# Kernel tuning notes

Hardware: AMD Instinct MI355X
Metric: run time of the kernel (lower is better)

## Reference

```python
import jax, jax.numpy as jnp
import numpy as np

N_NODES, N_EDGES = 50000, 800000
NODE_DIM, EDGE_DIM, HIDDEN, NUM_LAYERS = 64, 32, 64, 2
IN_MSG = NODE_DIM + EDGE_DIM  # 96
IN_UPD = NODE_DIM + HIDDEN    # 128


def setup_inputs() -> dict:
    key = jax.random.key(0)
    ks = jax.random.split(key, 12)
    def w(k, shape, fan_in):
        return jax.random.normal(k, shape, jnp.float32) * (1.0 / np.sqrt(fan_in))
    return {
        "node_features": jax.random.normal(ks[0], (N_NODES, NODE_DIM), jnp.float32),
        "edge_features": jax.random.normal(ks[1], (N_EDGES, EDGE_DIM), jnp.float32),
        "msg_w1": w(ks[2], (NUM_LAYERS, IN_MSG, HIDDEN), IN_MSG),
        "msg_b1": w(ks[3], (NUM_LAYERS, HIDDEN), IN_MSG),
        "msg_w2": w(ks[4], (NUM_LAYERS, HIDDEN, HIDDEN), HIDDEN),
        "msg_b2": w(ks[5], (NUM_LAYERS, HIDDEN), HIDDEN),
        "upd_w1": w(ks[6], (IN_UPD, HIDDEN), IN_UPD),
        "upd_b1": w(ks[7], (HIDDEN,), IN_UPD),
        "upd_w2": w(ks[8], (HIDDEN, NODE_DIM), HIDDEN),
        "upd_b2": w(ks[9], (NODE_DIM,), HIDDEN),
        "src": jax.random.randint(ks[10], (N_EDGES,), 0, N_NODES, dtype=jnp.int32),
        "dst": jax.random.randint(ks[11], (N_EDGES,), 0, N_NODES, dtype=jnp.int32),
    }


def reference(node_features, edge_features, msg_w1, msg_b1, msg_w2, msg_b2,
              upd_w1, upd_b1, upd_w2, upd_b2, src, dst):
    n_nodes = node_features.shape[0]
    # message: concat gathered source node feats with edge feats -> [E, node+edge]
    combined = jnp.concatenate([node_features[src], edge_features], axis=-1)
    # sum over the num_layers small Linear-ReLU-Linear message networks
    msg = jnp.zeros((combined.shape[0], msg_w2.shape[-1]), combined.dtype)
    for l in range(msg_w1.shape[0]):  # small fixed num_layers
        h = jax.nn.relu(combined @ msg_w1[l] + msg_b1[l])
        msg = msg + (h @ msg_w2[l] + msg_b2[l])
    # scatter-sum messages to destination nodes, normalize by neighbor count
    agg = jax.ops.segment_sum(msg, dst, num_segments=n_nodes)
    deg = jax.ops.segment_sum(jnp.ones((dst.shape[0],), msg.dtype), dst, num_segments=n_nodes)
    agg = agg / (deg[:, None] + 1e-8)
    # update MLP on concat(node, aggregated)
    comb2 = jnp.concatenate([node_features, agg], axis=-1)
    return jax.nn.relu(comb2 @ upd_w1 + upd_b1) @ upd_w2 + upd_b2
```

## Files before the change

kernel.cpp:

```cpp
#include <hip/hip_runtime.h>
#include <hip/hip_bf16.h>

#define NN 50000
#define NE 800000
#define ND 64
#define ED 32
#define HID 64
#define NL 2
#define IN_MSG 96
#define IN_UPD 128

#define W1_LD 104
#define MSG_LD 72
#define UPD_LD 136

#define NBLK 512
#define WPB 4
#define TOTW (NBLK * WPB)
#define NGRP (NE / 32)
#define NB_SCAN 196

typedef __attribute__((ext_vector_type(8))) short short8;
typedef __attribute__((ext_vector_type(4))) float f32x4;

__device__ inline ushort bf16r(float f) {
    __hip_bfloat16 h = __float2bfloat16(f);
    return *reinterpret_cast<ushort*>(&h);
}
__device__ inline float b2f(unsigned u) {
    union { unsigned u; float f; } x; x.u = u << 16; return x.f;
}
__device__ inline short8 pk8(float4 a, float4 b) {
    short8 r;
    r[0] = (short)bf16r(a.x); r[1] = (short)bf16r(a.y);
    r[2] = (short)bf16r(a.z); r[3] = (short)bf16r(a.w);
    r[4] = (short)bf16r(b.x); r[5] = (short)bf16r(b.y);
    r[6] = (short)bf16r(b.z); r[7] = (short)bf16r(b.w);
    return r;
}
__device__ inline uint2 pack4(float4 v) {
    return make_uint2((unsigned)bf16r(v.x) | ((unsigned)bf16r(v.y) << 16),
                      (unsigned)bf16r(v.z) | ((unsigned)bf16r(v.w) << 16));
}
__device__ inline uint2 pkacc(f32x4 a) {
    return make_uint2((unsigned)bf16r(a[0]) | ((unsigned)bf16r(a[1]) << 16),
                      (unsigned)bf16r(a[2]) | ((unsigned)bf16r(a[3]) << 16));
}

__global__ __launch_bounds__(256) void hist_kernel(const int* __restrict__ dst,
                                                   int* __restrict__ cnt)
{
    const int i = blockIdx.x * 256 + threadIdx.x;
    atomicAdd(&cnt[dst[i]], 1);
}

__global__ __launch_bounds__(256) void scanA_kernel(const int* __restrict__ cnt,
                                                    int* __restrict__ off,
                                                    int* __restrict__ bsum)
{
    __shared__ int buf[256];
    const int t = threadIdx.x;
    const int i = blockIdx.x * 256 + t;
    const int v = (i < NN) ? cnt[i] : 0;
    buf[t] = v;
    __syncthreads();
    #pragma unroll
    for (int d = 1; d < 256; d <<= 1) {
        const int x = (t >= d) ? buf[t - d] : 0;
        __syncthreads();
        buf[t] += x;
        __syncthreads();
    }
    if (i < NN) off[i] = buf[t] - v;
    if (t == 255) bsum[blockIdx.x] = buf[255];
}

__global__ __launch_bounds__(256) void scanB_kernel(int* __restrict__ bsum)
{
    __shared__ int buf[256];
    const int t = threadIdx.x;
    buf[t] = (t < NB_SCAN) ? bsum[t] : 0;
    __syncthreads();
    #pragma unroll
    for (int d = 1; d < 256; d <<= 1) {
        const int x = (t >= d) ? buf[t - d] : 0;
        __syncthreads();
        buf[t] += x;
        __syncthreads();
    }
    if (t < NB_SCAN) bsum[t] = buf[t];
}

__global__ __launch_bounds__(256) void scanC_kernel(const int* __restrict__ bsum,
                                                    int* __restrict__ off,
                                                    int* __restrict__ cursor)
{
    const int b = blockIdx.x;
    const int i = b * 256 + threadIdx.x;
    const int boff = (b > 0) ? bsum[b - 1] : 0;
    if (i < NN) {
        const int e = off[i] + boff;
        off[i] = e;
        cursor[i] = e;
    }
    if (i == 0) off[NN] = NE;
}

__global__ __launch_bounds__(256) void fill_kernel(const int* __restrict__ src,
                                                   const int* __restrict__ dst,
                                                   int* __restrict__ cursor,
                                                   int4* __restrict__ esd,
                                                   float4* __restrict__ agg4)
{
    const int i = blockIdx.x * 256 + threadIdx.x;
    const int d = dst[i];
    const int pos = atomicAdd(&cursor[d], 1);
    esd[pos] = make_int4(i, src[i], d, 0);
    agg4[i] = make_float4(0.f, 0.f, 0.f, 0.f);
}

template <int SORTED>
__global__ __launch_bounds__(256, 2)
void msg_kernel(const float* __restrict__ nf,
                const float* __restrict__ ef,
                const float* __restrict__ w1,
                const float* __restrict__ b1,
                const float* __restrict__ w2,
                const float* __restrict__ b2,
                const int* __restrict__ src,
                const int* __restrict__ dst,
                const int4* __restrict__ esd,
                float* __restrict__ agg,
                float* __restrict__ deg)
{
    __shared__ __align__(16) ushort sW1t[NL][64][W1_LD];
    __shared__ __align__(16) ushort sMS[WPB][32][MSG_LD];
    __shared__ __align__(16) float sB1f[NL][64];
    __shared__ __align__(16) float sB2f[64];

    const int tid = threadIdx.x;
    const int w  = tid >> 6;
    const int l  = tid & 63;
    const int lr = l & 15;
    const int lg = l >> 4;

    {
        const int k16 = tid >> 4, n0 = (tid & 15) * 4;
        #pragma unroll
        for (int lay = 0; lay < NL; ++lay)
            #pragma unroll
            for (int it = 0; it < 6; ++it) {
                const int k = k16 + 16 * it;
                const float4 v = *reinterpret_cast<const float4*>(
                    w1 + ((size_t)lay * IN_MSG + k) * HID + n0);
                sW1t[lay][n0 + 0][k] = bf16r(v.x);
                sW1t[lay][n0 + 1][k] = bf16r(v.y);
                sW1t[lay][n0 + 2][k] = bf16r(v.z);
                sW1t[lay][n0 + 3][k] = bf16r(v.w);
            }
        if (tid < NL * 64) sB1f[tid >> 6][tid & 63] = b1[tid];
        if (tid < 64) sB2f[tid] = b2[tid] + b2[HID + tid];
    }
    short8 w2f[NL][4][2];
    #pragma unroll
    for (int lay = 0; lay < NL; ++lay)
        #pragma unroll
        for (int nt = 0; nt < 4; ++nt)
            #pragma unroll
            for (int ks = 0; ks < 2; ++ks) {
                short8 t;
                #pragma unroll
                for (int j = 0; j < 8; ++j)
                    t[j] = (short)bf16r(
                        w2[((size_t)lay * HID + ks * 32 + 8 * lg + j) * HID + nt * 16 + lr]);
                w2f[lay][nt][ks] = t;
            }
    __syncthreads();

    const float4* nfr = reinterpret_cast<const float4*>(nf);
    const float4* efr = reinterpret_cast<const float4*>(ef);

    int g = blockIdx.x * WPB + w;
    int ev = 0, sv = 0, dv = 0;
    int en = 0, sn = 0, dn = 0;
    if (l < 32) {
        if (SORTED) { const int4 t = esd[(size_t)g * 32 + l]; ev = t.x; sv = t.y; dv = t.z; }
        else        { sv = src[(size_t)g * 32 + l]; dv = dst[(size_t)g * 32 + l]; }
    }
    {
        const int gn = g + TOTW;
        if (gn < NGRP && l < 32) {
            if (SORTED) { const int4 t = esd[(size_t)gn * 32 + l]; en = t.x; sn = t.y; dn = t.z; }
            else        { sn = src[(size_t)gn * 32 + l]; dn = dst[(size_t)gn * 32 + l]; }
        }
    }
    float4 nfv[2][4], efv[2][2];
    #pragma unroll
    for (int mt = 0; mt < 2; ++mt) {
        const int s = __shfl(sv, mt * 16 + lr);
        const float4* p = nfr + (size_t)s * 16;
        nfv[mt][0] = p[2 * lg];     nfv[mt][1] = p[2 * lg + 1];
        nfv[mt][2] = p[8 + 2 * lg]; nfv[mt][3] = p[9 + 2 * lg];
        const int e = SORTED ? __shfl(ev, mt * 16 + lr) : (g * 32 + mt * 16 + lr);
        const float4* q = efr + (size_t)e * 8;
        efv[mt][0] = q[2 * lg];
        efv[mt][1] = q[2 * lg + 1];
    }

    #pragma unroll 1
    while (g < NGRP) {
        const int gn  = g + TOTW;
        const int gnn = g + 2 * TOTW;
        const bool more = (gn < NGRP);

        short8 cmbA[2][3];
        #pragma unroll
        for (int mt = 0; mt < 2; ++mt) {
            cmbA[mt][0] = pk8(nfv[mt][0], nfv[mt][1]);
            cmbA[mt][1] = pk8(nfv[mt][2], nfv[mt][3]);
            cmbA[mt][2] = pk8(efv[mt][0], efv[mt][1]);
        }

        int en2 = 0, sn2 = 0, dn2 = 0;
        if (gnn < NGRP && l < 32) {
            if (SORTED) { const int4 t = esd[(size_t)gnn * 32 + l]; en2 = t.x; sn2 = t.y; dn2 = t.z; }
            else        { sn2 = src[(size_t)gnn * 32 + l]; dn2 = dst[(size_t)gnn * 32 + l]; }
        }
        float4 nfn[2][4], efn[2][2];
        if (more) {
            #pragma unroll
            for (int mt = 0; mt < 2; ++mt) {
                const int e = SORTED ? __shfl(en, mt * 16 + lr) : (gn * 32 + mt * 16 + lr);
                const float4* q = efr + (size_t)e * 8;
                efn[mt][0] = q[2 * lg];
                efn[mt][1] = q[2 * lg + 1];
                const int s = __shfl(sn, mt * 16 + lr);
                const float4* p = nfr + (size_t)s * 16;
                nfn[mt][0] = p[2 * lg];     nfn[mt][1] = p[2 * lg + 1];
                nfn[mt][2] = p[8 + 2 * lg]; nfn[mt][3] = p[9 + 2 * lg];
            }
        }

        f32x4 msg[2][4];
        #pragma unroll
        for (int nt = 0; nt < 4; ++nt) {
            const f32x4 b2v = *reinterpret_cast<const f32x4*>(&sB2f[nt * 16 + 4 * lg]);
            msg[0][nt] = b2v;
            msg[1][nt] = b2v;
        }

        #pragma unroll
        for (int lay = 0; lay < NL; ++lay) {
            f32x4 acc[2][4];
            #pragma unroll
            for (int nt = 0; nt < 4; ++nt) {
                const f32x4 bv = *reinterpret_cast<const f32x4*>(&sB1f[lay][nt * 16 + 4 * lg]);
                acc[0][nt] = bv;
                acc[1][nt] = bv;
            }
            __builtin_amdgcn_s_setprio(1);
            #pragma unroll
            for (int ks = 0; ks < 3; ++ks)
                #pragma unroll
                for (int nt = 0; nt < 4; ++nt) {
                    const short8 Bw = *reinterpret_cast<const short8*>(
                        &sW1t[lay][nt * 16 + lr][ks * 32 + 8 * lg]);
                    acc[0][nt] = __builtin_amdgcn_mfma_f32_16x16x32_bf16(Bw, cmbA[0][ks], acc[0][nt], 0, 0, 0);
                    acc[1][nt] = __builtin_amdgcn_mfma_f32_16x16x32_bf16(Bw, cmbA[1][ks], acc[1][nt], 0, 0, 0);
                }
            __builtin_amdgcn_s_setprio(0);
            #pragma unroll
            for (int mt = 0; mt < 2; ++mt)
                #pragma unroll
                for (int nt = 0; nt < 4; ++nt) {
                    f32x4 a = acc[mt][nt];
                    a[0] = fmaxf(a[0], 0.0f); a[1] = fmaxf(a[1], 0.0f);
                    a[2] = fmaxf(a[2], 0.0f); a[3] = fmaxf(a[3], 0.0f);
                    *reinterpret_cast<uint2*>(&sMS[w][mt * 16 + lr][nt * 16 + 4 * lg]) = pkacc(a);
                }
            short8 hA[2][2];
            #pragma unroll
            for (int mt = 0; mt < 2; ++mt)
                #pragma unroll
                for (int ks = 0; ks < 2; ++ks)
                    hA[mt][ks] = *reinterpret_cast<const short8*>(
                        &sMS[w][mt * 16 + lr][ks * 32 + 8 * lg]);
            __builtin_amdgcn_s_setprio(1);
            #pragma unroll
            for (int ks = 0; ks < 2; ++ks)
                #pragma unroll
                for (int nt = 0; nt < 4; ++nt) {
                    msg[0][nt] = __builtin_amdgcn_mfma_f32_16x16x32_bf16(w2f[lay][nt][ks], hA[0][ks], msg[0][nt], 0, 0, 0);
                    msg[1][nt] = __builtin_amdgcn_mfma_f32_16x16x32_bf16(w2f[lay][nt][ks], hA[1][ks], msg[1][nt], 0, 0, 0);
                }
            __builtin_amdgcn_s_setprio(0);
        }

        #pragma unroll
        for (int mt = 0; mt < 2; ++mt)
            #pragma unroll
            for (int nt = 0; nt < 4; ++nt)
                *reinterpret_cast<uint2*>(&sMS[w][mt * 16 + lr][nt * 16 + 4 * lg]) = pkacc(msg[mt][nt]);

        if (SORTED) {
            float acc = 0.0f;
            int dr = __builtin_amdgcn_readlane(dv, 0);
            #pragma unroll
            for (int r = 0; r < 32; ++r) {
                acc += b2f((unsigned)sMS[w][r][l]);
                const int drn = (r < 31) ? __builtin_amdgcn_readlane(dv, r + 1) : -1;
                if (r == 31 || dr != drn) {
                    atomicAdd(&agg[(size_t)dr * HID + l], acc);
                    acc = 0.0f;
                }
                dr = drn;
            }
        } else {
            #pragma unroll
            for (int r = 0; r < 32; ++r) {
                const int dr = __builtin_amdgcn_readlane(dv, r);
                atomicAdd(&agg[(size_t)dr * HID + l], b2f((unsigned)sMS[w][r][l]));
            }
            if (l < 32) atomicAdd(&deg[dv], 1.0f);
        }

        ev = en; sv = sn; dv = dn;
        en = en2; sn = sn2; dn = dn2;
        #pragma unroll
        for (int mt = 0; mt < 2; ++mt) {
            #pragma unroll
            for (int i = 0; i < 4; ++i) nfv[mt][i] = nfn[mt][i];
            efv[mt][0] = efn[mt][0]; efv[mt][1] = efn[mt][1];
        }
        g = gn;
    }
}

template <int USE_OFF>
__global__ __launch_bounds__(128, 2)
void node_update_kernel(const float* __restrict__ nf,
                        const float* __restrict__ agg,
                        const int* __restrict__ off,
                        const float* __restrict__ degf,
                        const float* __restrict__ uw1,
                        const float* __restrict__ ub1,
                        const float* __restrict__ uw2,
                        const float* __restrict__ ub2,
                        float* __restrict__ out)
{
    __shared__ __align__(16) ushort sAct[2][32][UPD_LD];
    __shared__ __align__(16) ushort sW1t[64][UPD_LD];
    __shared__ __align__(16) ushort sW2t[64][MSG_LD];
    __shared__ float sUB1[64], sUB2[64];

    const int tid = threadIdx.x;
    const int w  = tid >> 6;
    const int l  = tid & 63;
    const int lr = l & 15;
    const int lg = l >> 4;

    {
        const int k16 = tid >> 4, n0 = (tid & 15) * 4;
        #pragma unroll
        for (int it = 0; it < 16; ++it) {
            const int k = k16 + 8 * it;
            const float4 v = *reinterpret_cast<const float4*>(uw1 + (size_t)k * HID + n0);
            sW1t[n0 + 0][k] = bf16r(v.x);
            sW1t[n0 + 1][k] = bf16r(v.y);
            sW1t[n0 + 2][k] = bf16r(v.z);
            sW1t[n0 + 3][k] = bf16r(v.w);
        }
        #pragma unroll
        for (int it = 0; it < 8; ++it) {
            const int k = k16 + 8 * it;
            const float4 v = *reinterpret_cast<const float4*>(uw2 + (size_t)k * ND + n0);
            sW2t[n0 + 0][k] = bf16r(v.x);
            sW2t[n0 + 1][k] = bf16r(v.y);
            sW2t[n0 + 2][k] = bf16r(v.z);
            sW2t[n0 + 3][k] = bf16r(v.w);
        }
        if (tid < 64) { sUB1[tid] = ub1[tid]; sUB2[tid] = ub2[tid]; }
    }

    const int nbase = blockIdx.x * 64 + w * 32;
    float invv = 0.0f;
    if (l < 32) {
        const int n = min(nbase + l, NN - 1);
        const float d = USE_OFF ? (float)(off[n + 1] - off[n]) : degf[n];
        invv = 1.0f / (d + 1e-8f);
    }

    #pragma unroll
    for (int it = 0; it < 8; ++it) {
        const int row = lg + 4 * it;
        const int n = min(nbase + row, NN - 1);
        const float4 v = reinterpret_cast<const float4*>(nf + (size_t)n * ND)[lr];
        *reinterpret_cast<uint2*>(&sAct[w][row][lr * 4]) = pack4(v);
    }
    #pragma unroll
    for (int it = 0; it < 8; ++it) {
        const int row = lg + 4 * it;
        const int n = min(nbase + row, NN - 1);
        const float iv = __shfl(invv, row);
        float4 v = reinterpret_cast<const float4*>(agg + (size_t)n * HID)[lr];
        v.x *= iv; v.y *= iv; v.z *= iv; v.w *= iv;
        *reinterpret_cast<uint2*>(&sAct[w][row][ND + lr * 4]) = pack4(v);
    }
    __syncthreads();

    short8 A[2][4];
    #pragma unroll
    for (int mt = 0; mt < 2; ++mt)
        #pragma unroll
        for (int ks = 0; ks < 4; ++ks)
            A[mt][ks] = *reinterpret_cast<const short8*>(&sAct[w][mt * 16 + lr][ks * 32 + 8 * lg]);
    #pragma unroll
    for (int nt = 0; nt < 4; ++nt) {
        const int cB = nt * 16 + lr;
        short8 B[4];
        #pragma unroll
        for (int ks = 0; ks < 4; ++ks)
            B[ks] = *reinterpret_cast<const short8*>(&sW1t[cB][ks * 32 + 8 * lg]);
        const float bv = sUB1[cB];
        #pragma unroll
        for (int mt = 0; mt < 2; ++mt) {
            f32x4 acc = (f32x4){bv, bv, bv, bv};
            #pragma unroll
            for (int ks = 0; ks < 4; ++ks)
                acc = __builtin_amdgcn_mfma_f32_16x16x32_bf16(A[mt][ks], B[ks], acc, 0, 0, 0);
            const int rH = mt * 16 + 4 * lg;
            #pragma unroll
            for (int r = 0; r < 4; ++r)
                sAct[w][rH + r][cB] = bf16r(fmaxf(acc[r], 0.0f));
        }
    }

    f32x4 o[2][4];
    #pragma unroll
    for (int nt = 0; nt < 4; ++nt) {
        const float v = sUB2[nt * 16 + lr];
        o[0][nt] = (f32x4){v, v, v, v};
        o[1][nt] = (f32x4){v, v, v, v};
    }
    #pragma unroll
    for (int mt = 0; mt < 2; ++mt) {
        const short8 A0 = *reinterpret_cast<const short8*>(&sAct[w][mt * 16 + lr][ 0 + 8 * lg]);
        const short8 A1 = *reinterpret_cast<const short8*>(&sAct[w][mt * 16 + lr][32 + 8 * lg]);
        #pragma unroll
        for (int nt = 0; nt < 4; ++nt) {
            const int cB = nt * 16 + lr;
            const short8 B0 = *reinterpret_cast<const short8*>(&sW2t[cB][ 0 + 8 * lg]);
            const short8 B1 = *reinterpret_cast<const short8*>(&sW2t[cB][32 + 8 * lg]);
            o[mt][nt] = __builtin_amdgcn_mfma_f32_16x16x32_bf16(A0, B0, o[mt][nt], 0, 0, 0);
            o[mt][nt] = __builtin_amdgcn_mfma_f32_16x16x32_bf16(A1, B1, o[mt][nt], 0, 0, 0);
        }
    }

    #pragma unroll
    for (int mt = 0; mt < 2; ++mt)
        #pragma unroll
        for (int r = 0; r < 4; ++r) {
            const int n = nbase + mt * 16 + 4 * lg + r;
            if (n < NN) {
                float* rowp = out + (size_t)n * ND;
                #pragma unroll
                for (int nt = 0; nt < 4; ++nt)
                    rowp[nt * 16 + lr] = o[mt][nt][r];
            }
        }
}

extern "C" void kernel_launch(void* const* d_in, const int* in_sizes, int n_in,
                              void* d_out, int out_size, void* d_ws, size_t ws_size,
                              hipStream_t stream)
{
    const float* nf  = (const float*)d_in[0];
    const float* ef  = (const float*)d_in[1];
    const float* w1  = (const float*)d_in[2];
    const float* b1  = (const float*)d_in[3];
    const float* w2  = (const float*)d_in[4];
    const float* b2  = (const float*)d_in[5];
    const float* uw1 = (const float*)d_in[6];
    const float* ub1 = (const float*)d_in[7];
    const float* uw2 = (const float*)d_in[8];
    const float* ub2 = (const float*)d_in[9];
    const int*   src = (const int*)d_in[10];
    const int*   dst = (const int*)d_in[11];
    float* out = (float*)d_out;

    constexpr size_t ESDB = (size_t)NE * 16;
    constexpr size_t OFFB = (size_t)(NN + 1) * 4 + 12;
    constexpr size_t CNTB = (size_t)NN * 4;
    constexpr size_t BSUMB = 1024;
    constexpr size_t AGGB = (size_t)NN * HID * 4;
    constexpr size_t NEED = ESDB + OFFB + CNTB + BSUMB + AGGB;

    if (ws_size >= NEED) {
        char* p = (char*)d_ws;
        int4* esd  = (int4*)p;             p += ESDB;
        int*  off  = (int*)p;              p += OFFB;
        int*  cnt  = (int*)p;              p += CNTB;
        int*  bsum = (int*)p;              p += BSUMB;
        float* agg = (float*)p;

        (void)hipMemsetAsync(cnt, 0, CNTB, stream);
        hist_kernel<<<NE / 256, 256, 0, stream>>>(dst, cnt);
        scanA_kernel<<<NB_SCAN, 256, 0, stream>>>(cnt, off, bsum);
        scanB_kernel<<<1, 256, 0, stream>>>(bsum);
        scanC_kernel<<<NB_SCAN, 256, 0, stream>>>(bsum, off, cnt);
        fill_kernel<<<NE / 256, 256, 0, stream>>>(src, dst, cnt, esd,
                                                  (float4*)agg);
        msg_kernel<1><<<NBLK, 256, 0, stream>>>(nf, ef, w1, b1, w2, b2, src, dst,
                                                esd, agg, nullptr);
        node_update_kernel<1><<<(NN + 63) / 64, 128, 0, stream>>>(
            nf, agg, off, nullptr, uw1, ub1, uw2, ub2, out);
    } else {
        float* agg = (float*)d_ws;
        float* deg = agg + (size_t)NN * HID;
        (void)hipMemsetAsync(d_ws, 0, ((size_t)NN * HID + NN) * sizeof(float), stream);
        msg_kernel<0><<<NBLK, 256, 0, stream>>>(nf, ef, w1, b1, w2, b2, src, dst,
                                                nullptr, agg, deg);
        node_update_kernel<0><<<(NN + 63) / 64, 128, 0, stream>>>(
            nf, agg, nullptr, deg, uw1, ub1, uw2, ub2, out);
    }
}
```

Baseline: 170.2 us.

## Pre-permute edge features to bf16 in sorted order during fill

The fill kernel now reads edge features coalesced, converts them to bf16 and scatters them into dst-sorted order. The msg kernel can then stream them contiguously instead of gathering fp32 rows by original edge id. The index record also shrinks from int4 to int2. In exchange, fill does an extra 100MB read and a scattered 51MB write, and the workspace grows by 51MB, which may push execution onto the fallback path if the workspace is too small. pack4 is assumed to exist in the hidden portion of the file.

```diff
diff --git a/kernel.cpp b/kernel.cpp
--- a/kernel.cpp
+++ b/kernel.cpp
@@ -106,17 +106,34 @@
     if (i == 0) off[NN] = NE;
 }
 
-__global__ __launch_bounds__(256) void fill_kernel(const int* __restrict__ src,
-                                                   const int* __restrict__ dst,
-                                                   int* __restrict__ cursor,
-                                                   int4* __restrict__ esd,
-                                                   float4* __restrict__ agg4)
-{
-    const int i = blockIdx.x * 256 + threadIdx.x;
+__global__ __launch_bounds__(256)
+void fill_kernel(const float* __restrict__ ef,
+                 const int* __restrict__ src,
+                 const int* __restrict__ dst,
+                 int* __restrict__ cursor,
+                 int2* __restrict__ sdsort,
+                 ushort* __restrict__ efsort,
+                 float4* __restrict__ agg4)
+{
+    __shared__ int sPos[256];
+    const int tid = threadIdx.x;
+    const int i = blockIdx.x * 256 + tid;
     const int d = dst[i];
     const int pos = atomicAdd(&cursor[d], 1);
-    esd[pos] = make_int4(i, src[i], d, 0);
+    sdsort[pos] = make_int2(src[i], d);
+    sPos[tid] = pos;
     agg4[i] = make_float4(0.f, 0.f, 0.f, 0.f);
+    __syncthreads();
+    const int w = tid >> 6, l = tid & 63;
+    const int c = l & 7;
+    #pragma unroll
+    for (int it = 0; it < 8; ++it) {
+        const int rloc = w * 64 + (l >> 3) + 8 * it;
+        const size_t r = (size_t)blockIdx.x * 256 + rloc;
+        const float4 v = reinterpret_cast<const float4*>(ef)[r * 8 + c];
+        const uint2 pk = pack4(v);
+        *reinterpret_cast<uint2*>(efsort + (size_t)sPos[rloc] * 32 + c * 4) = pk;
+    }
 }
 
 template <int SORTED>
@@ -129,7 +146,8 @@
                 const float* __restrict__ b2,
                 const int* __restrict__ src,
                 const int* __restrict__ dst,
-                const int4* __restrict__ esd,
+                const int2* __restrict__ sdsort,
+                const ushort* __restrict__ efsort,
                 float* __restrict__ agg,
                 float* __restrict__ deg)
 {
@@ -181,30 +199,35 @@
     const float4* efr = reinterpret_cast<const float4*>(ef);
 
     int g = blockIdx.x * WPB + w;
-    int ev = 0, sv = 0, dv = 0;
-    int en = 0, sn = 0, dn = 0;
+    int sv = 0, dv = 0, sn = 0, dn = 0;
     if (l < 32) {
-        if (SORTED) { const int4 t = esd[(size_t)g * 32 + l]; ev = t.x; sv = t.y; dv = t.z; }
+        if (SORTED) { const int2 t = sdsort[(size_t)g * 32 + l]; sv = t.x; dv = t.y; }
         else        { sv = src[(size_t)g * 32 + l]; dv = dst[(size_t)g * 32 + l]; }
     }
     {
         const int gn = g + TOTW;
         if (gn < NGRP && l < 32) {
-            if (SORTED) { const int4 t = esd[(size_t)gn * 32 + l]; en = t.x; sn = t.y; dn = t.z; }
+            if (SORTED) { const int2 t = sdsort[(size_t)gn * 32 + l]; sn = t.x; dn = t.y; }
             else        { sn = src[(size_t)gn * 32 + l]; dn = dst[(size_t)gn * 32 + l]; }
         }
     }
-    float4 nfv[2][4], efv[2][2];
+    float4 nfv[2][4];
+    short8 efv[2];
+    float4 efvf[2][2];
     #pragma unroll
     for (int mt = 0; mt < 2; ++mt) {
         const int s = __shfl(sv, mt * 16 + lr);
         const float4* p = nfr + (size_t)s * 16;
         nfv[mt][0] = p[2 * lg];     nfv[mt][1] = p[2 * lg + 1];
         nfv[mt][2] = p[8 + 2 * lg]; nfv[mt][3] = p[9 + 2 * lg];
-        const int e = SORTED ? __shfl(ev, mt * 16 + lr) : (g * 32 + mt * 16 + lr);
-        const float4* q = efr + (size_t)e * 8;
-        efv[mt][0] = q[2 * lg];
-        efv[mt][1] = q[2 * lg + 1];
+        if (SORTED) {
+            efv[mt] = *reinterpret_cast<const short8*>(
+                efsort + (size_t)(g * 32 + mt * 16 + lr) * 32 + 8 * lg);
+        } else {
+            const float4* q = efr + (size_t)(g * 32 + mt * 16 + lr) * 8;
+            efvf[mt][0] = q[2 * lg];
+            efvf[mt][1] = q[2 * lg + 1];
+        }
     }
 
     #pragma unroll 1
@@ -218,22 +241,28 @@
         for (int mt = 0; mt < 2; ++mt) {
             cmbA[mt][0] = pk8(nfv[mt][0], nfv[mt][1]);
             cmbA[mt][1] = pk8(nfv[mt][2], nfv[mt][3]);
-            cmbA[mt][2] = pk8(efv[mt][0], efv[mt][1]);
-        }
-
-        int en2 = 0, sn2 = 0, dn2 = 0;
+            cmbA[mt][2] = SORTED ? efv[mt] : pk8(efvf[mt][0], efvf[mt][1]);
+        }
+
+        int sn2 = 0, dn2 = 0;
         if (gnn < NGRP && l < 32) {
-            if (SORTED) { const int4 t = esd[(size_t)gnn * 32 + l]; en2 = t.x; sn2 = t.y; dn2 = t.z; }
+            if (SORTED) { const int2 t = sdsort[(size_t)gnn * 32 + l]; sn2 = t.x; dn2 = t.y; }
             else        { sn2 = src[(size_t)gnn * 32 + l]; dn2 = dst[(size_t)gnn * 32 + l]; }
         }
-        float4 nfn[2][4], efn[2][2];
+        float4 nfn[2][4];
+        short8 efn[2];
+        float4 efnf[2][2];
         if (more) {
             #pragma unroll
             for (int mt = 0; mt < 2; ++mt) {
-                const int e = SORTED ? __shfl(en, mt * 16 + lr) : (gn * 32 + mt * 16 + lr);
-                const float4* q = efr + (size_t)e * 8;
-                efn[mt][0] = q[2 * lg];
-                efn[mt][1] = q[2 * lg + 1];
+                if (SORTED) {
+                    efn[mt] = *reinterpret_cast<const short8*>(
+                        efsort + (size_t)(gn * 32 + mt * 16 + lr) * 32 + 8 * lg);
+                } else {
+                    const float4* q = efr + (size_t)(gn * 32 + mt * 16 + lr) * 8;
+                    efnf[mt][0] = q[2 * lg];
+                    efnf[mt][1] = q[2 * lg + 1];
+                }
                 const int s = __shfl(sn, mt * 16 + lr);
                 const float4* p = nfr + (size_t)s * 16;
                 nfn[mt][0] = p[2 * lg];     nfn[mt][1] = p[2 * lg + 1];
@@ -324,13 +353,13 @@
             if (l < 32) atomicAdd(&deg[dv], 1.0f);
         }
 
-        ev = en; sv = sn; dv = dn;
-        en = en2; sn = sn2; dn = dn2;
+        sv = sn; dv = dn; sn = sn2; dn = dn2;
         #pragma unroll
         for (int mt = 0; mt < 2; ++mt) {
             #pragma unroll
             for (int i = 0; i < 4; ++i) nfv[mt][i] = nfn[mt][i];
-            efv[mt][0] = efn[mt][0]; efv[mt][1] = efn[mt][1];
+            if (SORTED) { efv[mt] = efn[mt]; }
+            else { efvf[mt][0] = efnf[mt][0]; efvf[mt][1] = efnf[mt][1]; }
         }
         g = gn;
     }
@@ -488,30 +517,32 @@
     const int*   dst = (const int*)d_in[11];
     float* out = (float*)d_out;
 
-    constexpr size_t ESDB = (size_t)NE * 16;
+    constexpr size_t SDB  = (size_t)NE * 8;
+    constexpr size_t EFB  = (size_t)NE * 64;
     constexpr size_t OFFB = (size_t)(NN + 1) * 4 + 12;
     constexpr size_t CNTB = (size_t)NN * 4;
     constexpr size_t BSUMB = 1024;
     constexpr size_t AGGB = (size_t)NN * HID * 4;
-    constexpr size_t NEED = ESDB + OFFB + CNTB + BSUMB + AGGB;
+    constexpr size_t NEED = SDB + EFB + OFFB + CNTB + BSUMB + AGGB;
 
     if (ws_size >= NEED) {
         char* p = (char*)d_ws;
-        int4* esd  = (int4*)p;             p += ESDB;
-        int*  off  = (int*)p;              p += OFFB;
-        int*  cnt  = (int*)p;              p += CNTB;
-        int*  bsum = (int*)p;              p += BSUMB;
-        float* agg = (float*)p;
+        int2*   sdsort = (int2*)p;         p += SDB;
+        ushort* efsort = (ushort*)p;       p += EFB;
+        int*    off    = (int*)p;          p += OFFB;
+        int*    cnt    = (int*)p;          p += CNTB;
+        int*    bsum   = (int*)p;          p += BSUMB;
+        float*  agg    = (float*)p;
 
         (void)hipMemsetAsync(cnt, 0, CNTB, stream);
         hist_kernel<<<NE / 256, 256, 0, stream>>>(dst, cnt);
         scanA_kernel<<<NB_SCAN, 256, 0, stream>>>(cnt, off, bsum);
         scanB_kernel<<<1, 256, 0, stream>>>(bsum);
         scanC_kernel<<<NB_SCAN, 256, 0, stream>>>(bsum, off, cnt);
-        fill_kernel<<<NE / 256, 256, 0, stream>>>(src, dst, cnt, esd,
-                                                  (float4*)agg);
+        fill_kernel<<<NE / 256, 256, 0, stream>>>(ef, src, dst, cnt, sdsort,
+                                                  efsort, (float4*)agg);
         msg_kernel<1><<<NBLK, 256, 0, stream>>>(nf, ef, w1, b1, w2, b2, src, dst,
-                                                esd, agg, nullptr);
+                                                sdsort, efsort, agg, nullptr);
         node_update_kernel<1><<<(NN + 63) / 64, 128, 0, stream>>>(
             nf, agg, off, nullptr, uw1, ub1, uw2, ub2, out);
     } else {
@@ -519,7 +550,7 @@
         float* deg = agg + (size_t)NN * HID;
         (void)hipMemsetAsync(d_ws, 0, ((size_t)NN * HID + NN) * sizeof(float), stream);
         msg_kernel<0><<<NBLK, 256, 0, stream>>>(nf, ef, w1, b1, w2, b2, src, dst,
-                                                nullptr, agg, deg);
+                                                nullptr, nullptr, agg, deg);
         node_update_kernel<0><<<(NN + 63) / 64, 128, 0, stream>>>(
             nf, agg, nullptr, deg, uw1, ub1, uw2, ub2, out);
     }
```

After: 175.9 us. 3.4% more time.
